# Optimization experiments

Hardware: AMD Instinct MI355X
Metric: run time of the kernel (lower is better)

## Reference

```python
import jax, jax.numpy as jnp
import numpy as np

B, T, I, H, O = 256, 224, 224, 1024, 4

def setup_inputs() -> dict:
    key = jax.random.key(0)
    ks = jax.random.split(key, 7)
    s_ih = 1.0 / np.sqrt(H)
    return {
        "x": jax.random.normal(ks[0], (B, T, I), dtype=jnp.float32),
        "W_ih": jax.random.uniform(ks[1], (H, I), jnp.float32, -s_ih, s_ih),
        "W_hh": jax.random.uniform(ks[2], (H, H), jnp.float32, -s_ih, s_ih),
        "b_ih": jax.random.uniform(ks[3], (H,), jnp.float32, -s_ih, s_ih),
        "b_hh": jax.random.uniform(ks[4], (H,), jnp.float32, -s_ih, s_ih),
        "W_fc": jax.random.uniform(ks[5], (O, H), jnp.float32, -s_ih, s_ih),
        "b_fc": jax.random.uniform(ks[6], (O,), jnp.float32, -s_ih, s_ih),
    }

def reference(x, W_ih, W_hh, b_ih, b_hh, W_fc, b_fc):
    # x: (B, T, I) -> permute(1,0,2) -> (T, B, I) as in torch forward
    xs = jnp.transpose(x, (1, 0, 2))
    # Precompute input projection for all timesteps: (T, B, H)
    x_proj = jnp.einsum("tbi,hi->tbh", xs, W_ih) + b_ih
    bias_h = b_hh

    def step(h, xp):
        # torch nn.RNN (tanh): h_t = tanh(x W_ih^T + b_ih + h W_hh^T + b_hh)
        h_new = jnp.tanh(xp + h @ W_hh.T + bias_h)
        return h_new, None

    h0 = jnp.zeros((xs.shape[1], W_hh.shape[0]), dtype=x.dtype)
    h_last, _ = jax.lax.scan(step, h0, x_proj)
    # FC on final hidden state, then view(-1, outputs): (B, O)
    out = h_last @ W_fc.T + b_fc
    return out
```

## Files before the change

kernel.cpp:

```cpp
#include <hip/hip_runtime.h>
#include <hip/hip_bf16.h>
#include <cstddef>

#define BB 256
#define TT 224
#define II 224
#define HH 1024
#define OO 4

typedef __attribute__((ext_vector_type(8))) short short8;
typedef __attribute__((ext_vector_type(4))) float f32x4;
typedef unsigned short ushort_t;

__device__ __forceinline__ unsigned short bfbits(float v) {
    __hip_bfloat16 b = __float2bfloat16(v);
    union { __hip_bfloat16 b; unsigned short u; } cv; cv.b = b; return cv.u;
}
__device__ __forceinline__ float bffloat(unsigned short u) {
    union { unsigned short u; __hip_bfloat16 b; } cv; cv.u = u; return __bfloat162float(cv.b);
}

#define LD128(d, p)      asm volatile("global_load_dwordx4 %0, %1, off" : "=v"(d) : "v"(p) : "memory")
#define LD128_SYS(d, p)  asm volatile("global_load_dwordx4 %0, %1, off sc0 sc1" : "=v"(d) : "v"(p) : "memory")
#define STD_SYS(p, v)    asm volatile("global_store_dword %0, %1, off sc0 sc1" :: "v"(p), "v"(v) : "memory")
#define WAIT_VM(n) do { asm volatile("s_waitcnt vmcnt(" #n ")" ::: "memory"); __builtin_amdgcn_sched_barrier(0); } while (0)

__device__ __forceinline__ void stflag(unsigned* p, unsigned v) {
    asm volatile("global_store_dword %0, %1, off sc0 sc1" :: "v"(p), "v"(v) : "memory");
}
__device__ __forceinline__ unsigned ldflag(const unsigned* p) {
    unsigned v;
    asm volatile("global_load_dword %0, %1, off sc0 sc1\n\ts_waitcnt vmcnt(0)"
                 : "=v"(v) : "v"(p) : "memory");
    return v;
}

__device__ __forceinline__ float fast_tanh(float v) {
    v = fminf(fmaxf(v, -15.f), 15.f);
    const float e = __expf(-2.f * v);
    return (1.f - e) * __builtin_amdgcn_rcpf(1.f + e);
}

#define MFMA(a, b, c) __builtin_amdgcn_mfma_f32_16x16x32_bf16(a, b, c, 0, 0, 0)

__global__ void zero_kernel(float* __restrict__ p, int n) {
    int i = blockIdx.x * blockDim.x + threadIdx.x;
    if (i < n) p[i] = 0.f;
}

__global__ __launch_bounds__(256) void split_hi_lo(
    const float* __restrict__ src, ushort_t* __restrict__ hi,
    ushort_t* __restrict__ lo, int n4)
{
    struct u4 { ushort_t v[4]; };
    const int stride = gridDim.x * blockDim.x;
    for (int i = blockIdx.x * blockDim.x + threadIdx.x; i < n4; i += stride) {
        float4 s = ((const float4*)src)[i];
        float vv[4] = {s.x, s.y, s.z, s.w};
        u4 h, l;
        #pragma unroll
        for (int j = 0; j < 4; ++j) {
            unsigned short hb = bfbits(vv[j]);
            h.v[j] = hb;
            l.v[j] = bfbits(vv[j] - bffloat(hb));
        }
        ((u4*)hi)[i] = h;
        ((u4*)lo)[i] = l;
    }
}

__global__ __launch_bounds__(512, 2) void rnn_persist8(
    const ushort_t* __restrict__ xh,   const ushort_t* __restrict__ xl,
    const ushort_t* __restrict__ wihh, const ushort_t* __restrict__ wihl,
    const ushort_t* __restrict__ whhh, const ushort_t* __restrict__ whhl,
    ushort_t* h0, ushort_t* h1, ushort_t* h2, ushort_t* h3,
    const float* __restrict__ b_ih, const float* __restrict__ b_hh,
    float* __restrict__ h32, unsigned* __restrict__ flags)
{
    __shared__ float red[2][8][16][66];

    const int tid = threadIdx.x;
    const int wv = tid >> 6, lane = tid & 63;
    const int row16 = lane & 15, kblk = lane >> 4;
    const int lid = blockIdx.x;
    const int rb = lid & 15;
    const int cb = lid >> 4;
    const int r0 = rb * 16, c0 = cb * 64;

    short8 wh[4][4], wl[4][4];
    #pragma unroll
    for (int n = 0; n < 4; ++n) {
        const ushort_t* bh = whhh + (size_t)(c0 + n * 16 + row16) * HH + 128 * wv + kblk * 8;
        const ushort_t* bl = whhl + (size_t)(c0 + n * 16 + row16) * HH + 128 * wv + kblk * 8;
        LD128(wh[n][0], bh);      LD128(wh[n][1], bh + 32);
        LD128(wh[n][2], bh + 64); LD128(wh[n][3], bh + 96);
        LD128(wl[n][0], bl);      LD128(wl[n][1], bl + 32);
        LD128(wl[n][2], bl + 64); LD128(wl[n][3], bl + 96);
    }
    WAIT_VM(0);

    const int erow = tid >> 5;
    const int ecp  = tid & 31;
    const int cg0  = c0 + 2 * ecp;
    const float bias0 = b_ih[cg0] + b_hh[cg0];
    const float bias1 = b_ih[cg0 + 1] + b_hh[cg0 + 1];

    const size_t ha = (size_t)(r0 + row16) * HH + 128 * wv + kblk * 8;
    const size_t xrow = (size_t)(r0 + row16) * TT;
    const size_t xcol = (size_t)wv * 32 + kblk * 8;

    const int cbp = 2 * wv + (lane >> 3);
    const int pwv = lane & 7;
    const unsigned* fp = (lane < 16)
        ? flags + (((size_t)(cbp * 16 + rb) * 8 + pwv) << 4)
        : flags;
    unsigned* ourflag = flags + (((size_t)lid * 8 + wv) << 4);

    for (int t = 0; t < TT; ++t) {
        const int rp = t & 3, wp = (t + 1) & 3;
        const ushort_t* hph = (rp & 2) ? ((rp & 1) ? h3 : h2) : ((rp & 1) ? h1 : h0);
        ushort_t*       hnh = (wp & 2) ? ((wp & 1) ? h3 : h2) : ((wp & 1) ? h1 : h0);

        short8 fxh{}, fxl{}, wih_[4], wil_[4];
        if (wv < 7) {
            LD128(fxh, xh + (xrow + t) * II + xcol);
            LD128(fxl, xl + (xrow + t) * II + xcol);
            #pragma unroll
            for (int n = 0; n < 4; ++n) {
                LD128(wih_[n], wihh + (size_t)(c0 + n * 16 + row16) * II + xcol);
                LD128(wil_[n], wihl + (size_t)(c0 + n * 16 + row16) * II + xcol);
            }
        }

        if (t) {
            while (true) {
                unsigned vf = ldflag(fp);
                const int ok = (lane < 16) ? (vf >= (unsigned)t) : 1;
                if (__ballot(ok) == ~0ull) break;
                __builtin_amdgcn_s_sleep(1);
            }
        }

        short8 fh[4];
        {
            const ushort_t* ph = hph + ha;
            LD128_SYS(fh[0], ph);
            LD128_SYS(fh[1], ph + 32);
            LD128_SYS(fh[2], ph + 64);
            LD128_SYS(fh[3], ph + 96);
        }

        f32x4 acc[4] = {};
        if (wv < 7) {
            WAIT_VM(4);
            #pragma unroll
            for (int n = 0; n < 4; ++n) {
                acc[n] = MFMA(fxh, wih_[n], acc[n]);
                acc[n] = MFMA(fxh, wil_[n], acc[n]);
                acc[n] = MFMA(fxl, wih_[n], acc[n]);
            }
        }
        __builtin_amdgcn_s_setprio(1);
        WAIT_VM(2);
        #pragma unroll
        for (int kb = 0; kb < 2; ++kb)
            #pragma unroll
            for (int n = 0; n < 4; ++n) {
                acc[n] = MFMA(fh[kb], wh[n][kb], acc[n]);
                acc[n] = MFMA(fh[kb], wl[n][kb], acc[n]);
            }
        WAIT_VM(0);
        #pragma unroll
        for (int kb = 2; kb < 4; ++kb)
            #pragma unroll
            for (int n = 0; n < 4; ++n) {
                acc[n] = MFMA(fh[kb], wh[n][kb], acc[n]);
                acc[n] = MFMA(fh[kb], wl[n][kb], acc[n]);
            }
        __builtin_amdgcn_s_setprio(0);

        #pragma unroll
        for (int n = 0; n < 4; ++n)
            #pragma unroll
            for (int jj = 0; jj < 4; ++jj)
                red[t & 1][wv][kblk * 4 + jj][n * 16 + row16] = acc[n][jj];
        __syncthreads();

        {
            float v0 = bias0, v1 = bias1;
            #pragma unroll
            for (int w = 0; w < 8; ++w) {
                float2 rv = *(const float2*)&red[t & 1][w][erow][2 * ecp];
                v0 += rv.x; v1 += rv.y;
            }
            v0 = fast_tanh(v0);
            v1 = fast_tanh(v1);
            const size_t o = (size_t)(r0 + erow) * HH + cg0;
            const unsigned short hb0 = bfbits(v0), hb1 = bfbits(v1);
            const unsigned packh = (unsigned)hb0 | ((unsigned)hb1 << 16);
            STD_SYS(hnh + o, packh);
            if (t == TT - 1) { h32[o] = v0; h32[o + 1] = v1; }
        }

        WAIT_VM(0);
        if (lane == 0) stflag(ourflag, (unsigned)(t + 1));
    }
}

__global__ __launch_bounds__(512) void rnn_step_f(
    const ushort_t* __restrict__ xh,   const ushort_t* __restrict__ xl,
    const ushort_t* __restrict__ wihh, const ushort_t* __restrict__ wihl,
    const ushort_t* __restrict__ whhh, const ushort_t* __restrict__ whhl,
    const ushort_t* __restrict__ hph,  ushort_t* __restrict__ hnh,
    const float* __restrict__ b_ih, const float* __restrict__ b_hh,
    float* __restrict__ h32, int t)
{
    __shared__ float red[8][16][66];
    const int tid = threadIdx.x;
    const int wv = tid >> 6, lane = tid & 63;
    const int row16 = lane & 15, kblk = lane >> 4;
    const int lid = blockIdx.x;
    const int rb = lid & 15, cb = lid >> 4;
    const int r0 = rb * 16, c0 = cb * 64;
    const size_t xcol = (size_t)wv * 32 + kblk * 8;

    f32x4 acc[4] = {};
    if (wv < 7) {
        const size_t xo = ((size_t)(r0 + row16) * TT + t) * II + xcol;
        short8 fxh = *(const short8*)(xh + xo);
        short8 fxl = *(const short8*)(xl + xo);
        #pragma unroll
        for (int n = 0; n < 4; ++n) {
            const size_t wo = (size_t)(c0 + n * 16 + row16) * II + xcol;
            short8 wiH = *(const short8*)(wihh + wo);
            short8 wiL = *(const short8*)(wihl + wo);
            acc[n] = MFMA(fxh, wiH, acc[n]);
            acc[n] = MFMA(fxh, wiL, acc[n]);
            acc[n] = MFMA(fxl, wiH, acc[n]);
        }
    }
    const size_t ha = (size_t)(r0 + row16) * HH + 128 * wv + kblk * 8;
    #pragma unroll
    for (int kb = 0; kb < 4; ++kb) {
        short8 fH = *(const short8*)(hph + ha + kb * 32);
        #pragma unroll
        for (int n = 0; n < 4; ++n) {
            const size_t wo = (size_t)(c0 + n * 16 + row16) * HH + 128 * wv + kb * 32 + kblk * 8;
            short8 wH = *(const short8*)(whhh + wo);
            short8 wL = *(const short8*)(whhl + wo);
            acc[n] = MFMA(fH, wH, acc[n]);
            acc[n] = MFMA(fH, wL, acc[n]);
        }
    }
    #pragma unroll
    for (int n = 0; n < 4; ++n)
        #pragma unroll
        for (int jj = 0; jj < 4; ++jj)
            red[wv][kblk * 4 + jj][n * 16 + row16] = acc[n][jj];
    __syncthreads();
    {
        const int erow = tid >> 5;
        const int ecp  = tid & 31;
        const int cg0  = c0 + 2 * ecp;
        float v0 = b_ih[cg0] + b_hh[cg0];
        float v1 = b_ih[cg0 + 1] + b_hh[cg0 + 1];
        #pragma unroll
        for (int w = 0; w < 8; ++w) {
            float2 rv = *(const float2*)&red[w][erow][2 * ecp];
            v0 += rv.x; v1 += rv.y;
        }
        v0 = tanhf(v0); v1 = tanhf(v1);
        const size_t o = (size_t)(r0 + erow) * HH + cg0;
        hnh[o] = bfbits(v0);  hnh[o + 1] = bfbits(v1);
        if (t == TT - 1) { h32[o] = v0; h32[o + 1] = v1; }
    }
}

__global__ __launch_bounds__(256) void fc_kernel(
    const float* __restrict__ h, const float* __restrict__ W_fc,
    const float* __restrict__ b_fc, float* __restrict__ out)
{
    const int b = blockIdx.x;
    const int tid = threadIdx.x;
    float p[OO] = {0.f, 0.f, 0.f, 0.f};
    for (int k = tid; k < HH; k += 256) {
        float hv = h[(size_t)b * HH + k];
        #pragma unroll
        for (int o = 0; o < OO; ++o) p[o] += hv * W_fc[(size_t)o * HH + k];
    }
    #pragma unroll
    for (int off = 32; off > 0; off >>= 1) {
        #pragma unroll
        for (int o = 0; o < OO; ++o) p[o] += __shfl_down(p[o], off, 64);
    }
    __shared__ float red[4][OO];
    const int wave = tid >> 6, lane = tid & 63;
    if (lane == 0) {
        #pragma unroll
        for (int o = 0; o < OO; ++o) red[wave][o] = p[o];
    }
    __syncthreads();
    if (tid < OO) {
        float s = red[0][tid] + red[1][tid] + red[2][tid] + red[3][tid] + b_fc[tid];
        out[b * OO + tid] = s;
    }
}

extern "C" void kernel_launch(void* const* d_in, const int* in_sizes, int n_in,
                              void* d_out, int out_size, void* d_ws, size_t ws_size,
                              hipStream_t stream) {
    const float* x    = (const float*)d_in[0];
    const float* W_ih = (const float*)d_in[1];
    const float* W_hh = (const float*)d_in[2];
    const float* b_ih = (const float*)d_in[3];
    const float* b_hh = (const float*)d_in[4];
    const float* W_fc = (const float*)d_in[5];
    const float* b_fc = (const float*)d_in[6];
    float* out = (float*)d_out;

    const size_t SZ_X   = (size_t)BB * TT * II * 2;
    const size_t SZ_WIH = (size_t)HH * II * 2;
    const size_t SZ_WHH = (size_t)HH * HH * 2;
    const size_t SZ_H   = (size_t)BB * HH * 2;
    const size_t OFF_XH   = 0;
    const size_t OFF_XL   = OFF_XH + SZ_X;
    const size_t OFF_WIHH = OFF_XL + SZ_X;
    const size_t OFF_WIHL = OFF_WIHH + SZ_WIH;
    const size_t OFF_WHHH = OFF_WIHL + SZ_WIH;
    const size_t OFF_WHHL = OFF_WHHH + SZ_WHH;
    const size_t OFF_H0   = OFF_WHHL + SZ_WHH;
    const size_t OFF_H32  = OFF_H0 + 4 * SZ_H;
    const size_t OFF_FLAGS = OFF_H32 + (size_t)BB * HH * 4;
    const size_t NEED      = OFF_FLAGS + 256 * 8 * 64;

    char* ws = (char*)d_ws;

    if (ws_size >= NEED) {
        ushort_t* xhp  = (ushort_t*)(ws + OFF_XH);
        ushort_t* xlp  = (ushort_t*)(ws + OFF_XL);
        ushort_t* wihh = (ushort_t*)(ws + OFF_WIHH);
        ushort_t* wihl = (ushort_t*)(ws + OFF_WIHL);
        ushort_t* whhh = (ushort_t*)(ws + OFF_WHHH);
        ushort_t* whhl = (ushort_t*)(ws + OFF_WHHL);
        ushort_t* hq[4];
        for (int i = 0; i < 4; ++i) hq[i] = (ushort_t*)(ws + OFF_H0 + (size_t)i * SZ_H);
        float*    h32  = (float*)(ws + OFF_H32);
        unsigned* flags = (unsigned*)(ws + OFF_FLAGS);

        split_hi_lo<<<1024, 256, 0, stream>>>(x, xhp, xlp, (BB * TT * II) / 4);
        split_hi_lo<<<128, 256, 0, stream>>>(W_ih, wihh, wihl, (HH * II) / 4);
        split_hi_lo<<<512, 256, 0, stream>>>(W_hh, whhh, whhl, (HH * HH) / 4);
        zero_kernel<<<(int)((SZ_H / 4 + 255) / 256), 256, 0, stream>>>((float*)(ws + OFF_H0), (int)(SZ_H / 4));
        zero_kernel<<<128, 256, 0, stream>>>((float*)flags, 256 * 8 * 16);

        const float* bihp = b_ih;
        const float* bhhp = b_hh;
        void* args[] = {
            (void*)&xhp, (void*)&xlp, (void*)&wihh, (void*)&wihl,
            (void*)&whhh, (void*)&whhl,
            (void*)&hq[0], (void*)&hq[1], (void*)&hq[2], (void*)&hq[3],
            (void*)&bihp, (void*)&bhhp, (void*)&h32, (void*)&flags
        };
        hipError_t e = hipLaunchCooperativeKernel((void*)rnn_persist8,
                                                  dim3(256), dim3(512), args, 0, stream);
        if (e != hipSuccess) {
            for (int t = 0; t < TT; ++t) {
                const int rp = t & 3, wp = (t + 1) & 3;
                rnn_step_f<<<256, 512, 0, stream>>>(
                    xhp, xlp, wihh, wihl, whhh, whhl,
                    hq[rp], hq[wp], b_ih, b_hh, h32, t);
            }
        }
        fc_kernel<<<BB, 256, 0, stream>>>(h32, W_fc, b_fc, out);
    }
}
```

Before: 943.9 us.

## Replace per-wave flag sync with sentinel-filled per-timestep hidden-state planes

```diff
diff --git a/kernel.cpp b/kernel.cpp
--- a/kernel.cpp
+++ b/kernel.cpp
@@ -7,9 +7,11 @@
 #define II 224
 #define HH 1024
 #define OO 4
+#define HPLANE ((size_t)BB * HH)
 
 typedef __attribute__((ext_vector_type(8))) short short8;
 typedef __attribute__((ext_vector_type(4))) float f32x4;
+typedef __attribute__((ext_vector_type(4))) unsigned uintx4;
 typedef unsigned short ushort_t;
 
 __device__ __forceinline__ unsigned short bfbits(float v) {
@@ -25,16 +27,6 @@
 #define STD_SYS(p, v)    asm volatile("global_store_dword %0, %1, off sc0 sc1" :: "v"(p), "v"(v) : "memory")
 #define WAIT_VM(n) do { asm volatile("s_waitcnt vmcnt(" #n ")" ::: "memory"); __builtin_amdgcn_sched_barrier(0); } while (0)
 
-__device__ __forceinline__ void stflag(unsigned* p, unsigned v) {
-    asm volatile("global_store_dword %0, %1, off sc0 sc1" :: "v"(p), "v"(v) : "memory");
-}
-__device__ __forceinline__ unsigned ldflag(const unsigned* p) {
-    unsigned v;
-    asm volatile("global_load_dword %0, %1, off sc0 sc1\n\ts_waitcnt vmcnt(0)"
-                 : "=v"(v) : "v"(p) : "memory");
-    return v;
-}
-
 __device__ __forceinline__ float fast_tanh(float v) {
     v = fminf(fmaxf(v, -15.f), 15.f);
     const float e = __expf(-2.f * v);
@@ -46,6 +38,13 @@
 __global__ void zero_kernel(float* __restrict__ p, int n) {
     int i = blockIdx.x * blockDim.x + threadIdx.x;
     if (i < n) p[i] = 0.f;
+}
+
+__global__ void fill_sentinel(uintx4* __restrict__ p, size_t n4) {
+    size_t i = (size_t)blockIdx.x * blockDim.x + threadIdx.x;
+    const size_t stride = (size_t)gridDim.x * blockDim.x;
+    const uintx4 s = {0xFFFFFFFFu, 0xFFFFFFFFu, 0xFFFFFFFFu, 0xFFFFFFFFu};
+    for (; i < n4; i += stride) p[i] = s;
 }
 
 __global__ __launch_bounds__(256) void split_hi_lo(
@@ -69,13 +68,13 @@
     }
 }
 
-__global__ __launch_bounds__(512, 2) void rnn_persist8(
+__global__ __launch_bounds__(512, 2) void rnn_persist9(
     const ushort_t* __restrict__ xh,   const ushort_t* __restrict__ xl,
     const ushort_t* __restrict__ wihh, const ushort_t* __restrict__ wihl,
     const ushort_t* __restrict__ whhh, const ushort_t* __restrict__ whhl,
-    ushort_t* h0, ushort_t* h1, ushort_t* h2, ushort_t* h3,
+    ushort_t* __restrict__ hbuf,
     const float* __restrict__ b_ih, const float* __restrict__ b_hh,
-    float* __restrict__ h32, unsigned* __restrict__ flags)
+    float* __restrict__ h32)
 {
     __shared__ float red[2][8][16][66];
 
@@ -109,17 +108,9 @@
     const size_t xrow = (size_t)(r0 + row16) * TT;
     const size_t xcol = (size_t)wv * 32 + kblk * 8;
 
-    const int cbp = 2 * wv + (lane >> 3);
-    const int pwv = lane & 7;
-    const unsigned* fp = (lane < 16)
-        ? flags + (((size_t)(cbp * 16 + rb) * 8 + pwv) << 4)
-        : flags;
-    unsigned* ourflag = flags + (((size_t)lid * 8 + wv) << 4);
-
     for (int t = 0; t < TT; ++t) {
-        const int rp = t & 3, wp = (t + 1) & 3;
-        const ushort_t* hph = (rp & 2) ? ((rp & 1) ? h3 : h2) : ((rp & 1) ? h1 : h0);
-        ushort_t*       hnh = (wp & 2) ? ((wp & 1) ? h3 : h2) : ((wp & 1) ? h1 : h0);
+        const ushort_t* hph = hbuf + (size_t)t * HPLANE;
+        ushort_t*       hnh = hbuf + (size_t)(t + 1) * HPLANE;
 
         short8 fxh{}, fxl{}, wih_[4], wil_[4];
         if (wv < 7) {
@@ -132,27 +123,33 @@
             }
         }
 
-        if (t) {
-            while (true) {
-                unsigned vf = ldflag(fp);
-                const int ok = (lane < 16) ? (vf >= (unsigned)t) : 1;
-                if (__ballot(ok) == ~0ull) break;
-                __builtin_amdgcn_s_sleep(1);
-            }
-        }
-
         short8 fh[4];
         {
             const ushort_t* ph = hph + ha;
-            LD128_SYS(fh[0], ph);
-            LD128_SYS(fh[1], ph + 32);
-            LD128_SYS(fh[2], ph + 64);
-            LD128_SYS(fh[3], ph + 96);
+            if (t) {
+                while (true) {
+                    LD128_SYS(fh[0], ph);      LD128_SYS(fh[1], ph + 32);
+                    LD128_SYS(fh[2], ph + 64); LD128_SYS(fh[3], ph + 96);
+                    WAIT_VM(0);
+                    unsigned ok = 1u;
+                    #pragma unroll
+                    for (int k = 0; k < 4; ++k) {
+                        uintx4 q = __builtin_bit_cast(uintx4, fh[k]);
+                        ok &= (q[0] != 0xFFFFFFFFu) & (q[1] != 0xFFFFFFFFu) &
+                              (q[2] != 0xFFFFFFFFu) & (q[3] != 0xFFFFFFFFu);
+                    }
+                    if (__ballot(ok) == ~0ull) break;
+                    __builtin_amdgcn_s_sleep(1);
+                }
+            } else {
+                LD128_SYS(fh[0], ph);      LD128_SYS(fh[1], ph + 32);
+                LD128_SYS(fh[2], ph + 64); LD128_SYS(fh[3], ph + 96);
+                WAIT_VM(0);
+            }
         }
 
         f32x4 acc[4] = {};
         if (wv < 7) {
-            WAIT_VM(4);
             #pragma unroll
             for (int n = 0; n < 4; ++n) {
                 acc[n] = MFMA(fxh, wih_[n], acc[n]);
@@ -161,17 +158,8 @@
             }
         }
         __builtin_amdgcn_s_setprio(1);
-        WAIT_VM(2);
-        #pragma unroll
-        for (int kb = 0; kb < 2; ++kb)
-            #pragma unroll
-            for (int n = 0; n < 4; ++n) {
-                acc[n] = MFMA(fh[kb], wh[n][kb], acc[n]);
-                acc[n] = MFMA(fh[kb], wl[n][kb], acc[n]);
-            }
-        WAIT_VM(0);
-        #pragma unroll
-        for (int kb = 2; kb < 4; ++kb)
+        #pragma unroll
+        for (int kb = 0; kb < 4; ++kb)
             #pragma unroll
             for (int n = 0; n < 4; ++n) {
                 acc[n] = MFMA(fh[kb], wh[n][kb], acc[n]);
@@ -201,9 +189,6 @@
             STD_SYS(hnh + o, packh);
             if (t == TT - 1) { h32[o] = v0; h32[o + 1] = v1; }
         }
-
-        WAIT_VM(0);
-        if (lane == 0) stflag(ourflag, (unsigned)(t + 1));
     }
 }
 
@@ -318,20 +303,19 @@
     const float* b_fc = (const float*)d_in[6];
     float* out = (float*)d_out;
 
-    const size_t SZ_X   = (size_t)BB * TT * II * 2;
-    const size_t SZ_WIH = (size_t)HH * II * 2;
-    const size_t SZ_WHH = (size_t)HH * HH * 2;
-    const size_t SZ_H   = (size_t)BB * HH * 2;
+    const size_t SZ_X    = (size_t)BB * TT * II * 2;
+    const size_t SZ_WIH  = (size_t)HH * II * 2;
+    const size_t SZ_WHH  = (size_t)HH * HH * 2;
+    const size_t SZ_HP   = HPLANE * 2;
     const size_t OFF_XH   = 0;
     const size_t OFF_XL   = OFF_XH + SZ_X;
     const size_t OFF_WIHH = OFF_XL + SZ_X;
     const size_t OFF_WIHL = OFF_WIHH + SZ_WIH;
     const size_t OFF_WHHH = OFF_WIHL + SZ_WIH;
     const size_t OFF_WHHL = OFF_WHHH + SZ_WHH;
-    const size_t OFF_H0   = OFF_WHHL + SZ_WHH;
-    const size_t OFF_H32  = OFF_H0 + 4 * SZ_H;
-    const size_t OFF_FLAGS = OFF_H32 + (size_t)BB * HH * 4;
-    const size_t NEED      = OFF_FLAGS + 256 * 8 * 64;
+    const size_t OFF_HBUF = OFF_WHHL + SZ_WHH;
+    const size_t OFF_H32  = OFF_HBUF + (size_t)(TT + 1) * SZ_HP;
+    const size_t NEED     = OFF_H32 + (size_t)BB * HH * 4;
 
     char* ws = (char*)d_ws;
 
@@ -342,33 +326,31 @@
         ushort_t* wihl = (ushort_t*)(ws + OFF_WIHL);
         ushort_t* whhh = (ushort_t*)(ws + OFF_WHHH);
         ushort_t* whhl = (ushort_t*)(ws + OFF_WHHL);
-        ushort_t* hq[4];
-        for (int i = 0; i < 4; ++i) hq[i] = (ushort_t*)(ws + OFF_H0 + (size_t)i * SZ_H);
+        ushort_t* hbuf = (ushort_t*)(ws + OFF_HBUF);
         float*    h32  = (float*)(ws + OFF_H32);
-        unsigned* flags = (unsigned*)(ws + OFF_FLAGS);
 
         split_hi_lo<<<1024, 256, 0, stream>>>(x, xhp, xlp, (BB * TT * II) / 4);
         split_hi_lo<<<128, 256, 0, stream>>>(W_ih, wihh, wihl, (HH * II) / 4);
         split_hi_lo<<<512, 256, 0, stream>>>(W_hh, whhh, whhl, (HH * HH) / 4);
-        zero_kernel<<<(int)((SZ_H / 4 + 255) / 256), 256, 0, stream>>>((float*)(ws + OFF_H0), (int)(SZ_H / 4));
-        zero_kernel<<<128, 256, 0, stream>>>((float*)flags, 256 * 8 * 16);
+        zero_kernel<<<(int)((SZ_HP / 4 + 255) / 256), 256, 0, stream>>>((float*)hbuf, (int)(SZ_HP / 4));
+        fill_sentinel<<<2048, 256, 0, stream>>>((uintx4*)(hbuf + HPLANE),
+                                                (size_t)TT * SZ_HP / 16);
 
         const float* bihp = b_ih;
         const float* bhhp = b_hh;
         void* args[] = {
             (void*)&xhp, (void*)&xlp, (void*)&wihh, (void*)&wihl,
-            (void*)&whhh, (void*)&whhl,
-            (void*)&hq[0], (void*)&hq[1], (void*)&hq[2], (void*)&hq[3],
-            (void*)&bihp, (void*)&bhhp, (void*)&h32, (void*)&flags
+            (void*)&whhh, (void*)&whhl, (void*)&hbuf,
+            (void*)&bihp, (void*)&bhhp, (void*)&h32
         };
-        hipError_t e = hipLaunchCooperativeKernel((void*)rnn_persist8,
+        hipError_t e = hipLaunchCooperativeKernel((void*)rnn_persist9,
                                                   dim3(256), dim3(512), args, 0, stream);
         if (e != hipSuccess) {
             for (int t = 0; t < TT; ++t) {
-                const int rp = t & 3, wp = (t + 1) & 3;
                 rnn_step_f<<<256, 512, 0, stream>>>(
                     xhp, xlp, wihh, wihl, whhh, whhl,
-                    hq[rp], hq[wp], b_ih, b_hh, h32, t);
+                    hbuf + (size_t)t * HPLANE, hbuf + (size_t)(t + 1) * HPLANE,
+                    b_ih, b_hh, h32, t);
             }
         }
         fc_kernel<<<BB, 256, 0, stream>>>(h32, W_fc, b_fc, out);
```

Measured after the change: 855.5 us. 9.4% less time.
